# Kernel optimization log

Hardware: AMD Instinct MI355X
Metric: run time of the kernel (lower is better)

The kernel has to match this reference:

```python
import jax, jax.numpy as jnp
import numpy as np

B, C, T, V, D, H, KT = 64, 3, 256, 21, 128, 4, 9


def _adjacency():
    rng = np.random.default_rng(0)
    Araw = (rng.random((V, V)) < 0.3).astype(np.float32)
    Araw = np.maximum(Araw, Araw.T)
    np.fill_diagonal(Araw, 1.0)
    deg = Araw.sum(1)
    Anorm = Araw / np.sqrt(deg[:, None] * deg[None, :])  # D^-1/2 A D^-1/2
    return Araw.astype(np.float32), Anorm.astype(np.float32)


def setup_inputs() -> dict:
    key = jax.random.key(0)
    ks = jax.random.split(key, 24)
    g = lambda i, shape, sc=0.05: jax.random.normal(ks[i], shape, dtype=jnp.float32) * sc
    Araw, Anorm = _adjacency()
    return {
        'x': jax.random.normal(ks[0], (B, C, T, V), dtype=jnp.float32),
        'coord_w': g(1, (C, D)), 'coord_b': g(2, (D,)),
        'joint_emb': g(3, (V, D)),
        'graph_bias': jnp.asarray(Araw),  # nn.Parameter(A.clone().float())
        'wq': g(4, (D, D)), 'bq': g(5, (D,)),
        'wk': g(6, (D, D)), 'bk': g(7, (D,)),
        'wv': g(8, (D, D)), 'bv': g(9, (D,)),
        'wo': g(10, (D, D)), 'bo': g(11, (D,)),
        'gcn_w1': g(12, (D, D)), 'gcn_b1': g(13, (D,)),
        'tcn_w1': g(14, (D, D, KT, 1)), 'tcn_b1': g(15, (D,)),
        'gcn_w2': g(16, (D, D)), 'gcn_b2': g(17, (D,)),
        'tcn_w2': g(18, (D, D, KT, 1)), 'tcn_b2': g(19, (D,)),
        'A': jnp.asarray(Anorm),  # fixed normalized adjacency buffer
    }


def _stgcn(x, A, gw, gb, tw, tb):
    # x: [B, D, T, V]; spatial graph conv then temporal conv, residual.
    res = x
    y = jnp.einsum('bctv,vw->bctw', x, A)              # neighbor aggregation
    y = jnp.einsum('bctv,dc->bdtv', y, gw) + gb[None, :, None, None]
    y = jax.nn.relu(y)
    y = jax.lax.conv_general_dilated(
        y, tw, window_strides=(1, 1), padding=((KT // 2, KT // 2), (0, 0)),
        dimension_numbers=('NCHW', 'OIHW', 'NCHW'))     # temporal conv, kernel 9
    y = y + tb[None, :, None, None]
    return jax.nn.relu(y + res)


def reference(x, coord_w, coord_b, joint_emb, graph_bias, wq, bq, wk, bk, wv, bv,
              wo, bo, gcn_w1, gcn_b1, tcn_w1, tcn_b1, gcn_w2, gcn_b2, tcn_w2,
              tcn_b2, A):
    b, c, t, v = x.shape
    d = coord_w.shape[1]
    dh = d // H
    scale = jnp.float32(1.0 / np.sqrt(dh))
    coords = x.transpose(0, 2, 3, 1).reshape(b * t, v, c)      # [N, V, 3]
    feat = coords @ coord_w + coord_b + joint_emb              # LearnedJointEncoding
    q = (feat @ wq + bq).reshape(-1, v, H, dh)
    k = (feat @ wk + bk).reshape(-1, v, H, dh)
    val = (feat @ wv + bv).reshape(-1, v, H, dh)
    scores = jnp.einsum('nihd,njhd->nhij', q, k) * scale + graph_bias[None, None]
    attn = jax.nn.softmax(scores, axis=-1)                     # [N, H, V, V]
    out = jnp.einsum('nhij,njhd->nihd', attn, val).reshape(-1, v, d)
    feat = out @ wo + bo
    feat = feat.reshape(b, t, v, d).transpose(0, 3, 1, 2)       # [B, D, T, V]
    feat = _stgcn(feat, A, gcn_w1, gcn_b1, tcn_w1, tcn_b1)
    feat = _stgcn(feat, A, gcn_w2, gcn_b2, tcn_w2, tcn_b2)
    return feat, attn
```

## Files before the change

### kernel.cpp

```cpp
#include <hip/hip_runtime.h>
#include <hip/hip_bf16.h>

typedef __hip_bfloat16 bf16;
typedef __attribute__((ext_vector_type(8))) short short8v;
typedef __attribute__((ext_vector_type(4))) float float4v;

#define BB   64
#define CC   3
#define TLEN 256
#define VJ   21
#define DM   128
#define NH   4
#define DH   32
#define KT   9
#define NFR  (BB*TLEN)
#define MTOK (NFR*VJ)
#define NIN  22

__device__ __forceinline__ float b2f(bf16 x){ return __bfloat162float(x); }
__device__ __forceinline__ bf16  f2b(float x){ return __float2bfloat16(x); }
__device__ __forceinline__ float hb2f(short s){ return __uint_as_float(((unsigned)(unsigned short)s) << 16); }
__device__ __forceinline__ float lo16(unsigned u){ return __uint_as_float(u << 16); }
__device__ __forceinline__ float hi16(unsigned u){ return __uint_as_float(u & 0xffff0000u); }

__global__ void detect_dtype(const void* __restrict__ xin, int nus, int* __restrict__ flag){
  const unsigned short* u = (const unsigned short*)xin;
  int lim = nus < 65536 ? nus : 65536;
  int bad = 0;
  for (int k = threadIdx.x; k < lim; k += 256){
    float f = __uint_as_float(((unsigned)u[k]) << 16);
    if (!(fabsf(f) < 1e6f)) bad = 1;
  }
  if (bad) atomicOr(flag, 1);
}

struct ConvArgs { const void* src[NIN]; int off[NIN+1]; };

__global__ void convert_inputs(ConvArgs a, bf16* __restrict__ dst,
                               const int* __restrict__ flag, int total){
  int i = blockIdx.x*256 + threadIdx.x;
  if (i >= total) return;
  bool isf32 = (*flag != 0);
  int k = 0;
  while (i >= a.off[k+1]) ++k;
  int j = i - a.off[k];
  float v;
  if (isf32) v = ((const float*)a.src[k])[j];
  else       v = __uint_as_float(((unsigned)((const unsigned short*)a.src[k])[j]) << 16);
  dst[i] = f2b(v);
}

__global__ void prep_weights(const bf16* __restrict__ wq, const bf16* __restrict__ wk,
                             const bf16* __restrict__ wv, const bf16* __restrict__ wo,
                             const bf16* __restrict__ tw1, const bf16* __restrict__ tw2,
                             bf16* __restrict__ wqT, bf16* __restrict__ wkT,
                             bf16* __restrict__ wvT, bf16* __restrict__ woT,
                             bf16* __restrict__ twT1, bf16* __restrict__ twT2){
  int i = blockIdx.x*256 + threadIdx.x;
  if (i < DM*DM){
    int d = i >> 7, e = i & 127;
    wqT[i] = wq[e*DM + d];
    wkT[i] = wk[e*DM + d];
    wvT[i] = wv[e*DM + d];
    woT[i] = wo[e*DM + d];
  }
  if (i < KT*DM*DM){
    int c = i & 127; int d = (i >> 7) & 127; int tap = i >> 14;
    twT1[i] = tw1[(d*DM + c)*KT + tap];
    twT2[i] = tw2[(d*DM + c)*KT + tap];
  }
}

__global__ __launch_bounds__(256) void encode_kernel(const bf16* __restrict__ x,
                                                     const bf16* __restrict__ cw,
                                                     const bf16* __restrict__ cb,
                                                     const bf16* __restrict__ je,
                                                     bf16* __restrict__ feat){
  int idx = blockIdx.x*256 + threadIdx.x;
  if (idx >= MTOK*16) return;
  int d0 = (idx & 15) * 8;
  int n  = idx >> 4;
  int v  = n % VJ; int t = (n / VJ) % TLEN; int b = n / (VJ*TLEN);
  float xs[CC];
  #pragma unroll
  for (int c = 0; c < CC; ++c)
    xs[c] = b2f(x[((size_t)(b*CC + c)*TLEN + t)*VJ + v]);
  short8v cwv[CC];
  #pragma unroll
  for (int c = 0; c < CC; ++c)
    cwv[c] = *reinterpret_cast<const short8v*>(cw + c*DM + d0);
  short8v cbv = *reinterpret_cast<const short8v*>(cb + d0);
  short8v jev = *reinterpret_cast<const short8v*>(je + v*DM + d0);
  short8v out;
  #pragma unroll
  for (int e = 0; e < 8; ++e){
    float acc = hb2f(cbv[e]) + hb2f(jev[e]);
    #pragma unroll
    for (int c = 0; c < CC; ++c) acc = fmaf(xs[c], hb2f(cwv[c][e]), acc);
    bf16 h = f2b(acc);
    out[e] = *reinterpret_cast<short*>(&h);
  }
  *reinterpret_cast<short8v*>(feat + (size_t)n*DM + d0*1) = out;
}

__global__ __launch_bounds__(512) void qkv_gemm(const bf16* __restrict__ A,
                                                const bf16* __restrict__ BtQ,
                                                const bf16* __restrict__ BtK,
                                                const bf16* __restrict__ BtV,
                                                const bf16* __restrict__ bq,
                                                const bf16* __restrict__ bk,
                                                const bf16* __restrict__ bv,
                                                bf16* __restrict__ Oq,
                                                bf16* __restrict__ Ok,
                                                bf16* __restrict__ Ov){
  __shared__ short8v lds[128*16];
  const int tid = threadIdx.x;
  const int r0  = blockIdx.x*128;
  for (int i = tid; i < 128*16; i += 512){
    int row = i >> 4, c0 = i & 15;
    lds[row*16 + (c0 ^ (row & 7))] = *reinterpret_cast<const short8v*>(A + ((size_t)r0 + row)*DM + c0*8);
  }
  __syncthreads();
  const int lane = tid & 63;
  const int wid  = tid >> 6;
  const int rbase = (wid >> 2) * 64;
  const int nt0   = (wid & 3) * 2;
  const int l15 = lane & 15, l4 = lane >> 4;
  #pragma unroll
  for (int w = 0; w < 3; ++w){
    const bf16* Bt  = (w==0) ? BtQ : (w==1) ? BtK : BtV;
    const bf16* bia = (w==0) ? bq  : (w==1) ? bk  : bv;
    bf16*       Out = (w==0) ? Oq  : (w==1) ? Ok  : Ov;
    short8v breg[2][4];
    #pragma unroll
    for (int ntl = 0; ntl < 2; ++ntl)
      #pragma unroll
      for (int ks = 0; ks < 4; ++ks)
        breg[ntl][ks] = *reinterpret_cast<const short8v*>(Bt + ((nt0+ntl)*16 + l15)*DM + ks*32 + l4*8);
    float4v acc[4][2];
    #pragma unroll
    for (int rt = 0; rt < 4; ++rt){ acc[rt][0] = (float4v){0,0,0,0}; acc[rt][1] = (float4v){0,0,0,0}; }
    #pragma unroll
    for (int rt = 0; rt < 4; ++rt){
      const int ldsRow = rbase + rt*16 + l15;
      #pragma unroll
      for (int ks = 0; ks < 4; ++ks){
        short8v a = lds[ldsRow*16 + ((ks*4 + l4) ^ (ldsRow & 7))];
        acc[rt][0] = __builtin_amdgcn_mfma_f32_16x16x32_bf16(a, breg[0][ks], acc[rt][0], 0,0,0);
        acc[rt][1] = __builtin_amdgcn_mfma_f32_16x16x32_bf16(a, breg[1][ks], acc[rt][1], 0,0,0);
      }
    }
    #pragma unroll
    for (int rt = 0; rt < 4; ++rt)
      #pragma unroll
      for (int ntl = 0; ntl < 2; ++ntl){
        int col = (nt0+ntl)*16 + l15;
        float bvv = b2f(bia[col]);
        #pragma unroll
        for (int j = 0; j < 4; ++j)
          Out[(size_t)(r0 + rbase + rt*16 + l4*4 + j)*DM + col] = f2b(acc[rt][ntl][j] + bvv);
      }
  }
}

template<int NTAPS, bool RELU, bool RESID>
__global__ __launch_bounds__(512) void conv_gemm(const bf16* __restrict__ A,
                                                 const bf16* __restrict__ Bt,
                                                 const bf16* __restrict__ bias,
                                                 const bf16* resid,
                                                 bf16* Cout){
  constexpr int HALO = (NTAPS/2)*VJ;
  constexpr int ROWS = 128 + 2*HALO;
  __shared__ short8v lds[ROWS*16];
  const int tid = threadIdx.x;
  const int r0  = blockIdx.x*128;
  for (int i = tid; i < ROWS*16; i += 512){
    int row = i >> 4, c0 = i & 15;
    long tok = (long)r0 - HALO + row;
    if (tok < 0) tok = 0;
    if (tok > MTOK-1) tok = MTOK-1;
    lds[row*16 + (c0 ^ (row & 7))] = *reinterpret_cast<const short8v*>(A + tok*DM + c0*8);
  }
  __syncthreads();
  const int lane = tid & 63;
  const int wid  = tid >> 6;
  const int rbase = (wid >> 2) * 64;
  const int nt0   = (wid & 3) * 2;
  const int l15 = lane & 15, l4 = lane >> 4;
  int trow[4];
  #pragma unroll
  for (int rt = 0; rt < 4; ++rt)
    trow[rt] = ((r0 + rbase + rt*16 + l15) / VJ) % TLEN;
  float4v acc[4][2];
  #pragma unroll
  for (int rt = 0; rt < 4; ++rt){ acc[rt][0] = (float4v){0,0,0,0}; acc[rt][1] = (float4v){0,0,0,0}; }

  for (int tap = 0; tap < NTAPS; ++tap){
    const bf16* Btap = Bt + (size_t)tap*DM*DM;
    short8v breg[2][4];
    #pragma unroll
    for (int ntl = 0; ntl < 2; ++ntl)
      #pragma unroll
      for (int ks = 0; ks < 4; ++ks)
        breg[ntl][ks] = *reinterpret_cast<const short8v*>(Btap + ((nt0+ntl)*16 + l15)*DM + ks*32 + l4*8);
    #pragma unroll
    for (int rt = 0; rt < 4; ++rt){
      bool valid = true;
      if (NTAPS > 1){
        int ts = trow[rt] + tap - NTAPS/2;
        valid = (ts >= 0) && (ts < TLEN);
      }
      const int ldsRow = rbase + rt*16 + l15 + HALO + (tap - NTAPS/2)*VJ;
      #pragma unroll
      for (int ks = 0; ks < 4; ++ks){
        short8v a = lds[ldsRow*16 + ((ks*4 + l4) ^ (ldsRow & 7))];
        if (NTAPS > 1 && !valid) a = (short8v){0,0,0,0,0,0,0,0};
        acc[rt][0] = __builtin_amdgcn_mfma_f32_16x16x32_bf16(a, breg[0][ks], acc[rt][0], 0,0,0);
        acc[rt][1] = __builtin_amdgcn_mfma_f32_16x16x32_bf16(a, breg[1][ks], acc[rt][1], 0,0,0);
      }
    }
  }
  #pragma unroll
  for (int rt = 0; rt < 4; ++rt){
    #pragma unroll
    for (int ntl = 0; ntl < 2; ++ntl){
      int col = (nt0+ntl)*16 + l15;
      float bv = b2f(bias[col]);
      #pragma unroll
      for (int j = 0; j < 4; ++j){
        size_t idx = (size_t)(r0 + rbase + rt*16 + l4*4 + j)*DM + col;
        float val = acc[rt][ntl][j] + bv;
        if (RESID) val += b2f(resid[idx]);
        if (RELU) val = fmaxf(val, 0.f);
        Cout[idx] = f2b(val);
      }
    }
  }
}

__global__ __launch_bounds__(256) void attn_core(const bf16* __restrict__ Q,
                                                 const bf16* __restrict__ K,
                                                 const bf16* __restrict__ V,
                                                 const bf16* __restrict__ gbias,
                                                 float* __restrict__ attn_out,
                                                 bf16* __restrict__ ao_out){
  const int n = blockIdx.x;
  const int tid = threadIdx.x;
  __shared__ bf16 skv[3][VJ][136];
  __shared__ float sc[NH*VJ*VJ];
  __shared__ float rmax[NH*VJ], rinv[NH*VJ];
  __shared__ bf16 sgb[VJ*VJ];

  for (int i = tid; i < VJ*VJ; i += 256) sgb[i] = gbias[i];
  for (int i = tid; i < 3*VJ*16; i += 256){
    int c0 = i & 15; int v = (i >> 4) % VJ; int w = i / (16*VJ);
    const bf16* src = (w==0 ? Q : (w==1 ? K : V)) + ((size_t)n*VJ + v)*DM + c0*8;
    *reinterpret_cast<short8v*>(&skv[w][v][c0*8]) = *reinterpret_cast<const short8v*>(src);
  }
  __syncthreads();
  const float scale = 0.17677669529663687f;
  for (int idx = tid; idx < NH*VJ*VJ; idx += 256){
    int j = idx % VJ, i2 = (idx/VJ) % VJ, h = idx/(VJ*VJ);
    const unsigned* qr = reinterpret_cast<const unsigned*>(&skv[0][i2][h*DH]);
    const unsigned* kr = reinterpret_cast<const unsigned*>(&skv[1][j][h*DH]);
    float a = 0.f;
    #pragma unroll
    for (int p = 0; p < DH/2; ++p){
      unsigned qa = qr[p], ka = kr[p];
      a = fmaf(lo16(qa), lo16(ka), a);
      a = fmaf(hi16(qa), hi16(ka), a);
    }
    sc[idx] = a*scale + b2f(sgb[i2*VJ + j]);
  }
  __syncthreads();
  for (int r = tid; r < NH*VJ; r += 256){
    float m = -1e30f;
    for (int j = 0; j < VJ; ++j) m = fmaxf(m, sc[r*VJ + j]);
    float s = 0.f;
    for (int j = 0; j < VJ; ++j) s += __expf(sc[r*VJ + j] - m);
    rmax[r] = m; rinv[r] = 1.0f/s;
  }
  __syncthreads();
  for (int idx = tid; idx < NH*VJ*VJ; idx += 256){
    int r = idx / VJ;
    float e = __expf(sc[idx] - rmax[r]) * rinv[r];
    sc[idx] = e;
    attn_out[(size_t)n*(NH*VJ*VJ) + idx] = e;
  }
  __syncthreads();
  unsigned* aoU = reinterpret_cast<unsigned*>(ao_out);
  for (int i = tid; i < VJ*(DM/2); i += 256){
    int q2 = i & 63; int v = i >> 6;
    int d0 = q2*2; int h = d0 >> 5;
    const float* pr = &sc[(h*VJ + v)*VJ];
    float a0 = 0.f, a1 = 0.f;
    #pragma unroll
    for (int j = 0; j < VJ; ++j){
      unsigned va = *reinterpret_cast<const unsigned*>(&skv[2][j][d0]);
      float p = pr[j];
      a0 = fmaf(p, lo16(va), a0);
      a1 = fmaf(p, hi16(va), a1);
    }
    bf16 b0 = f2b(a0), b1 = f2b(a1);
    unsigned u0 = *reinterpret_cast<unsigned short*>(&b0);
    unsigned u1 = *reinterpret_cast<unsigned short*>(&b1);
    aoU[((size_t)n*VJ + v)*(DM/2) + q2] = u0 | (u1 << 16);
  }
}

__global__ __launch_bounds__(256) void agg_kernel(const bf16* __restrict__ fin,
                                                  const bf16* __restrict__ An,
                                                  bf16* __restrict__ aout){
  const int n = blockIdx.x;
  const int tid = threadIdx.x;
  __shared__ bf16 sx[VJ][136];
  __shared__ float sA[VJ*VJ];
  for (int i = tid; i < VJ*VJ; i += 256) sA[i] = b2f(An[i]);
  for (int i = tid; i < VJ*16; i += 256){
    int c0 = i & 15, v = i >> 4;
    *reinterpret_cast<short8v*>(&sx[v][c0*8]) =
      *reinterpret_cast<const short8v*>(fin + ((size_t)n*VJ + v)*DM + c0*8);
  }
  __syncthreads();
  for (int i = tid; i < VJ*16; i += 256){
    int c0 = i & 15, w = i >> 4;
    float acc[8] = {0,0,0,0,0,0,0,0};
    #pragma unroll
    for (int u = 0; u < VJ; ++u){
      float a = sA[u*VJ + w];
      short8v xv = *reinterpret_cast<const short8v*>(&sx[u][c0*8]);
      #pragma unroll
      for (int e = 0; e < 8; ++e) acc[e] = fmaf(a, hb2f(xv[e]), acc[e]);
    }
    short8v out;
    #pragma unroll
    for (int e = 0; e < 8; ++e){ bf16 h = f2b(acc[e]); out[e] = *reinterpret_cast<short*>(&h); }
    *reinterpret_cast<short8v*>(aout + ((size_t)n*VJ + w)*DM + c0*8) = out;
  }
}

__global__ __launch_bounds__(256) void transpose_out(const bf16* __restrict__ fin,
                                                     float* __restrict__ fout){
  const int bid = blockIdx.x;
  const int b   = bid >> 5;
  const int rem = bid & 31;
  const int t0  = (rem >> 2) * 32;
  const int d0  = (rem & 3) * 32;
  __shared__ bf16 tile[32][VJ][33];
  const int tid = threadIdx.x;
  for (int idx = tid; idx < 32*VJ*32; idx += 256){
    int dl = idx & 31;
    int v  = (idx >> 5) % VJ;
    int tl = idx / (32*VJ);
    tile[tl][v][dl] = fin[((size_t)(b*TLEN + t0 + tl)*VJ + v)*DM + d0 + dl];
  }
  __syncthreads();
  for (int idx = tid; idx < 32*VJ*32; idx += 256){
    int j  = idx % (32*VJ);
    int dl = idx / (32*VJ);
    int tl = j / VJ, v = j % VJ;
    fout[((size_t)(b*DM + d0 + dl)*TLEN + t0 + tl)*VJ + v] = b2f(tile[tl][v][dl]);
  }
}

extern "C" void kernel_launch(void* const* d_in, const int* in_sizes, int n_in,
                              void* d_out, int out_size, void* d_ws, size_t ws_size,
                              hipStream_t stream){
  const size_t featElems = (size_t)MTOK*DM;
  float* outf    = (float*)d_out;
  float* attnOut = outf + featElems;
  bf16* qbuf = (bf16*)d_out;
  bf16* kbuf = qbuf + featElems;

  char* wp = (char*)d_ws;
  auto alloc = [&](size_t bytes)->char*{ char* p = wp; wp += (bytes + 15) & ~(size_t)15; return p; };
  int*  flag = (int*)alloc(16);
  ConvArgs ca; int total = 0;
  for (int i = 0; i < NIN; ++i){ ca.src[i] = d_in[i]; ca.off[i] = total; total += in_sizes[i]; }
  ca.off[NIN] = total;
  bf16* cin   = (bf16*)alloc((size_t)total*2);
  bf16* wqT   = (bf16*)alloc(DM*DM*2);
  bf16* wkT   = (bf16*)alloc(DM*DM*2);
  bf16* wvT   = (bf16*)alloc(DM*DM*2);
  bf16* woT   = (bf16*)alloc(DM*DM*2);
  bf16* twT1  = (bf16*)alloc(KT*DM*DM*2);
  bf16* twT2  = (bf16*)alloc(KT*DM*DM*2);
  bf16* featA = (bf16*)alloc(featElems*2);
  bf16* bufV  = (bf16*)alloc(featElems*2);
  if ((size_t)(wp - (char*)d_ws) > ws_size) return;

  const bf16* x    = cin + ca.off[0];
  const bf16* cw   = cin + ca.off[1];
  const bf16* cb   = cin + ca.off[2];
  const bf16* je   = cin + ca.off[3];
  const bf16* gbias= cin + ca.off[4];
  const bf16* wq   = cin + ca.off[5];
  const bf16* bq   = cin + ca.off[6];
  const bf16* wk   = cin + ca.off[7];
  const bf16* bk   = cin + ca.off[8];
  const bf16* wv   = cin + ca.off[9];
  const bf16* bv   = cin + ca.off[10];
  const bf16* wo   = cin + ca.off[11];
  const bf16* bo   = cin + ca.off[12];
  const bf16* gw1  = cin + ca.off[13];
  const bf16* gb1  = cin + ca.off[14];
  const bf16* tw1  = cin + ca.off[15];
  const bf16* tb1  = cin + ca.off[16];
  const bf16* gw2  = cin + ca.off[17];
  const bf16* gb2  = cin + ca.off[18];
  const bf16* tw2  = cin + ca.off[19];
  const bf16* tb2  = cin + ca.off[20];
  const bf16* An   = cin + ca.off[21];

  const int GB = MTOK/128;
  hipMemsetAsync(flag, 0, sizeof(int), stream);
  detect_dtype<<<1, 256, 0, stream>>>(d_in[0], in_sizes[0], flag);
  convert_inputs<<<(total + 255)/256, 256, 0, stream>>>(ca, cin, flag, total);
  prep_weights<<<(KT*DM*DM + 255)/256, 256, 0, stream>>>(wq, wk, wv, wo, tw1, tw2,
                                                         wqT, wkT, wvT, woT, twT1, twT2);
  encode_kernel<<<(MTOK*16 + 255)/256, 256, 0, stream>>>(x, cw, cb, je, featA);
  qkv_gemm<<<GB, 512, 0, stream>>>(featA, wqT, wkT, wvT, bq, bk, bv, qbuf, kbuf, bufV);
  attn_core<<<NFR, 256, 0, stream>>>(qbuf, kbuf, bufV, gbias, attnOut, featA);
  conv_gemm<1,false,false><<<GB, 512, 0, stream>>>(featA, woT, bo, nullptr, bufV);
  agg_kernel<<<NFR, 256, 0, stream>>>(bufV, An, qbuf);
  conv_gemm<1,true,false><<<GB, 512, 0, stream>>>(qbuf, gw1, gb1, nullptr, kbuf);
  conv_gemm<9,true,true><<<GB, 512, 0, stream>>>(kbuf, twT1, tb1, bufV, bufV);
  agg_kernel<<<NFR, 256, 0, stream>>>(bufV, An, qbuf);
  conv_gemm<1,true,false><<<GB, 512, 0, stream>>>(qbuf, gw2, gb2, nullptr, kbuf);
  conv_gemm<9,true,true><<<GB, 512, 0, stream>>>(kbuf, twT2, tb2, bufV, bufV);
  transpose_out<<<BB*(TLEN/32)*(DM/32), 256, 0, stream>>>(bufV, outf);
}
```

Baseline: 1.344 ms.

## Replace halo-tiled temporal conv with per-(batch,joint) full-sequence tap GEMM kernel

Temporal 9-tap convolution moves to a new kernel with one block per (batch, joint). Each block loads that joint's whole 256-step sequence into LDS and accumulates all 128 output channels over taps, so no halo rows are reloaded and the bias, residual and ReLU are fused at the end. The old conv_gemm is reduced to a single-tap GEMM with the halo and validity logic removed. The new kernel uses strided token gathers (stride of 21 tokens) and a large per-thread accumulator (128 floats), which may add register pressure and lower occupancy.

```diff
diff --git a/kernel.cpp b/kernel.cpp
--- a/kernel.cpp
+++ b/kernel.cpp
@@ -169,17 +169,12 @@
                                                  const bf16* __restrict__ bias,
                                                  const bf16* resid,
                                                  bf16* Cout){
-  constexpr int HALO = (NTAPS/2)*VJ;
-  constexpr int ROWS = 128 + 2*HALO;
-  __shared__ short8v lds[ROWS*16];
+  __shared__ short8v lds[128*16];
   const int tid = threadIdx.x;
   const int r0  = blockIdx.x*128;
-  for (int i = tid; i < ROWS*16; i += 512){
+  for (int i = tid; i < 128*16; i += 512){
     int row = i >> 4, c0 = i & 15;
-    long tok = (long)r0 - HALO + row;
-    if (tok < 0) tok = 0;
-    if (tok > MTOK-1) tok = MTOK-1;
-    lds[row*16 + (c0 ^ (row & 7))] = *reinterpret_cast<const short8v*>(A + tok*DM + c0*8);
+    lds[row*16 + (c0 ^ (row & 7))] = *reinterpret_cast<const short8v*>(A + ((size_t)r0 + row)*DM + c0*8);
   }
   __syncthreads();
   const int lane = tid & 63;
@@ -187,37 +182,23 @@
   const int rbase = (wid >> 2) * 64;
   const int nt0   = (wid & 3) * 2;
   const int l15 = lane & 15, l4 = lane >> 4;
-  int trow[4];
-  #pragma unroll
-  for (int rt = 0; rt < 4; ++rt)
-    trow[rt] = ((r0 + rbase + rt*16 + l15) / VJ) % TLEN;
   float4v acc[4][2];
   #pragma unroll
   for (int rt = 0; rt < 4; ++rt){ acc[rt][0] = (float4v){0,0,0,0}; acc[rt][1] = (float4v){0,0,0,0}; }
-
-  for (int tap = 0; tap < NTAPS; ++tap){
-    const bf16* Btap = Bt + (size_t)tap*DM*DM;
-    short8v breg[2][4];
-    #pragma unroll
-    for (int ntl = 0; ntl < 2; ++ntl)
-      #pragma unroll
-      for (int ks = 0; ks < 4; ++ks)
-        breg[ntl][ks] = *reinterpret_cast<const short8v*>(Btap + ((nt0+ntl)*16 + l15)*DM + ks*32 + l4*8);
-    #pragma unroll
-    for (int rt = 0; rt < 4; ++rt){
-      bool valid = true;
-      if (NTAPS > 1){
-        int ts = trow[rt] + tap - NTAPS/2;
-        valid = (ts >= 0) && (ts < TLEN);
-      }
-      const int ldsRow = rbase + rt*16 + l15 + HALO + (tap - NTAPS/2)*VJ;
-      #pragma unroll
-      for (int ks = 0; ks < 4; ++ks){
-        short8v a = lds[ldsRow*16 + ((ks*4 + l4) ^ (ldsRow & 7))];
-        if (NTAPS > 1 && !valid) a = (short8v){0,0,0,0,0,0,0,0};
-        acc[rt][0] = __builtin_amdgcn_mfma_f32_16x16x32_bf16(a, breg[0][ks], acc[rt][0], 0,0,0);
-        acc[rt][1] = __builtin_amdgcn_mfma_f32_16x16x32_bf16(a, breg[1][ks], acc[rt][1], 0,0,0);
-      }
+  short8v breg[2][4];
+  #pragma unroll
+  for (int ntl = 0; ntl < 2; ++ntl)
+    #pragma unroll
+    for (int ks = 0; ks < 4; ++ks)
+      breg[ntl][ks] = *reinterpret_cast<const short8v*>(Bt + ((nt0+ntl)*16 + l15)*DM + ks*32 + l4*8);
+  #pragma unroll
+  for (int rt = 0; rt < 4; ++rt){
+    const int ldsRow = rbase + rt*16 + l15;
+    #pragma unroll
+    for (int ks = 0; ks < 4; ++ks){
+      short8v a = lds[ldsRow*16 + ((ks*4 + l4) ^ (ldsRow & 7))];
+      acc[rt][0] = __builtin_amdgcn_mfma_f32_16x16x32_bf16(a, breg[0][ks], acc[rt][0], 0,0,0);
+      acc[rt][1] = __builtin_amdgcn_mfma_f32_16x16x32_bf16(a, breg[1][ks], acc[rt][1], 0,0,0);
     }
   }
   #pragma unroll
@@ -233,6 +214,68 @@
         if (RESID) val += b2f(resid[idx]);
         if (RELU) val = fmaxf(val, 0.f);
         Cout[idx] = f2b(val);
+      }
+    }
+  }
+}
+
+__global__ __launch_bounds__(256, 2) void tconv_bv(const bf16* __restrict__ Y,
+                                                   const bf16* __restrict__ twT,
+                                                   const bf16* __restrict__ bias,
+                                                   const bf16* resid,
+                                                   bf16* Cout){
+  __shared__ short8v lds[TLEN*16];
+  const int bid = blockIdx.x;
+  const int b = bid / VJ, v = bid % VJ;
+  const size_t tokBase = (size_t)b*TLEN*VJ + v;
+  const int tid = threadIdx.x;
+  for (int i = tid; i < TLEN*16; i += 256){
+    int t = i >> 4, c0 = i & 15;
+    lds[t*16 + (c0 ^ (t & 7))] =
+      *reinterpret_cast<const short8v*>(Y + (tokBase + (size_t)t*VJ)*DM + c0*8);
+  }
+  __syncthreads();
+  const int lane = tid & 63;
+  const int wr   = tid >> 6;
+  const int l15 = lane & 15, l4 = lane >> 4;
+  float4v acc[4][8];
+  #pragma unroll
+  for (int rt = 0; rt < 4; ++rt)
+    #pragma unroll
+    for (int ct = 0; ct < 8; ++ct) acc[rt][ct] = (float4v){0,0,0,0};
+
+  for (int tap = 0; tap < KT; ++tap){
+    const bf16* Btap = twT + (size_t)tap*DM*DM;
+    const int dt = tap - KT/2;
+    #pragma unroll
+    for (int ks = 0; ks < 4; ++ks){
+      short8v bfr[8];
+      #pragma unroll
+      for (int ct = 0; ct < 8; ++ct)
+        bfr[ct] = *reinterpret_cast<const short8v*>(Btap + (ct*16 + l15)*DM + ks*32 + l4*8);
+      #pragma unroll
+      for (int rt = 0; rt < 4; ++rt){
+        int ts = wr*64 + rt*16 + l15 + dt;
+        short8v a = {0,0,0,0,0,0,0,0};
+        if (ts >= 0 && ts < TLEN) a = lds[ts*16 + ((ks*4 + l4) ^ (ts & 7))];
+        #pragma unroll
+        for (int ct = 0; ct < 8; ++ct)
+          acc[rt][ct] = __builtin_amdgcn_mfma_f32_16x16x32_bf16(a, bfr[ct], acc[rt][ct], 0,0,0);
+      }
+    }
+  }
+  #pragma unroll
+  for (int rt = 0; rt < 4; ++rt){
+    #pragma unroll
+    for (int ct = 0; ct < 8; ++ct){
+      int col = ct*16 + l15;
+      float bv = b2f(bias[col]);
+      #pragma unroll
+      for (int j = 0; j < 4; ++j){
+        int t = wr*64 + rt*16 + l4*4 + j;
+        size_t idx = (tokBase + (size_t)t*VJ)*DM + col;
+        float val = acc[rt][ct][j] + bv + b2f(resid[idx]);
+        Cout[idx] = f2b(fmaxf(val, 0.f));
       }
     }
   }
@@ -424,9 +467,9 @@
   conv_gemm<1,false,false><<<GB, 512, 0, stream>>>(featA, woT, bo, nullptr, bufV);
   agg_kernel<<<NFR, 256, 0, stream>>>(bufV, An, qbuf);
   conv_gemm<1,true,false><<<GB, 512, 0, stream>>>(qbuf, gw1, gb1, nullptr, kbuf);
-  conv_gemm<9,true,true><<<GB, 512, 0, stream>>>(kbuf, twT1, tb1, bufV, bufV);
+  tconv_bv<<<BB*VJ, 256, 0, stream>>>(kbuf, twT1, tb1, bufV, bufV);
   agg_kernel<<<NFR, 256, 0, stream>>>(bufV, An, qbuf);
   conv_gemm<1,true,false><<<GB, 512, 0, stream>>>(qbuf, gw2, gb2, nullptr, kbuf);
-  conv_gemm<9,true,true><<<GB, 512, 0, stream>>>(kbuf, twT2, tb2, bufV, bufV);
+  tconv_bv<<<BB*VJ, 256, 0, stream>>>(kbuf, twT2, tb2, bufV, bufV);
   transpose_out<<<BB*(TLEN/32)*(DM/32), 256, 0, stream>>>(bufV, outf);
 }
```

Result: slower. 1.469 ms (+9.3%).
